# Optimization experiments

Hardware: AMD Instinct MI355X
Metric: run time of the kernel (lower is better)

Reference implementation:

```python
import jax, jax.numpy as jnp
import numpy as np

IN_F, OUT_F, GROUP = 4096, 11008, 128
NUM_GROUPS = IN_F // GROUP


def setup_inputs() -> dict:
    key = jax.random.key(0)
    k1, k2, k3, k4 = jax.random.split(key, 4)
    x = jax.random.normal(k1, (4, 2048, IN_F), dtype=jnp.float32)
    weight_q = jax.random.randint(k2, (OUT_F, IN_F), 0, 127, dtype=jnp.int32)
    scales = jax.random.uniform(k3, (OUT_F, NUM_GROUPS), dtype=jnp.float16) * jnp.float16(0.01)
    bias = jax.random.normal(k4, (OUT_F,), dtype=jnp.float32)
    return {"x": x, "weight_q": weight_q, "scales": scales, "bias": bias}


def _group_dequantize(weight_q, scales):
    # symmetric: W[o, g*G + j] = q[o, g*G + j] * scales[o, g]
    q = weight_q.astype(jnp.float32).reshape(OUT_F, NUM_GROUPS, GROUP)
    w = q * scales.astype(jnp.float32)[:, :, None]
    return w.reshape(OUT_F, IN_F)


def reference(x, weight_q, scales, bias):
    W = _group_dequantize(weight_q, scales).astype(x.dtype)  # [O, I]
    # F.linear: x @ W.T + bias
    out = jnp.einsum('bsi,oi->bso', x, W) + bias.astype(x.dtype)
    return out
```

## Files before the change

### kernel.cpp

```cpp
#include <hip/hip_runtime.h>
#include <hip/hip_fp16.h>

#define K_DIM   4096
#define N_DIM   11008
#define M_DIM   8192
#define NGROUPS 32

#define BM 128
#define BN 128
#define BK 64

typedef __bf16 bf16x8 __attribute__((ext_vector_type(8)));
typedef float  f32x4  __attribute__((ext_vector_type(4)));

#define GAS __attribute__((address_space(1)))
#define LAS __attribute__((address_space(3)))

__device__ __forceinline__ unsigned short f2bf(float f) {
    unsigned int u = __float_as_uint(f);
    u += 0x7fffu + ((u >> 16) & 1u);
    return (unsigned short)(u >> 16);
}

__global__ void prep_x_kernel(const float4* __restrict__ x, ushort4* __restrict__ xb, int nq) {
    int stride = gridDim.x * blockDim.x;
    for (int i = blockIdx.x * blockDim.x + threadIdx.x; i < nq; i += stride) {
        float4 v = x[i];
        ushort4 o;
        o.x = f2bf(v.x); o.y = f2bf(v.y); o.z = f2bf(v.z); o.w = f2bf(v.w);
        xb[i] = o;
    }
}

__global__ void prep_w_kernel(const int4* __restrict__ q, const float* __restrict__ sc,
                              ushort4* __restrict__ wb, int nq) {
    int stride = gridDim.x * blockDim.x;
    for (int i = blockIdx.x * blockDim.x + threadIdx.x; i < nq; i += stride) {
        int4 v = q[i];
        int o = i >> 10;
        int g = (i & 1023) >> 5;
        float s = sc[(o << 5) + g];
        ushort4 w;
        w.x = f2bf((float)v.x * s);
        w.y = f2bf((float)v.y * s);
        w.z = f2bf((float)v.z * s);
        w.w = f2bf((float)v.w * s);
        wb[i] = w;
    }
}

__global__ void gemm_bf16_kernel(const ushort* __restrict__ A, const ushort* __restrict__ B,
                                 const float* __restrict__ bias, float* __restrict__ C) {
    __shared__ __align__(16) ushort sA[BM * BK];
    __shared__ __align__(16) ushort sB[BN * BK];

    const int tid  = threadIdx.x;
    const int lane = tid & 63;
    const int wid  = tid >> 6;
    const int bn   = blockIdx.x;
    const int bm   = blockIdx.y;

    const ushort* Abase = A + (size_t)bm * BM * K_DIM;
    const ushort* Bbase = B + (size_t)bn * BN * K_DIM;

    int g_off[4];
#pragma unroll
    for (int q = 0; q < 4; ++q) {
        int slot = q * 256 + tid;
        int row  = slot >> 3;
        int g    = (slot & 7) ^ (row & 7);
        g_off[q] = row * K_DIM + g * 8;
    }
    const int lds_u = (tid & ~63) * 8;

    f32x4 acc[4][4];
#pragma unroll
    for (int i = 0; i < 4; ++i)
#pragma unroll
        for (int j = 0; j < 4; ++j) {
            acc[i][j][0] = 0.f; acc[i][j][1] = 0.f;
            acc[i][j][2] = 0.f; acc[i][j][3] = 0.f;
        }

    const int mw = (wid & 1) * 64;
    const int nw = (wid >> 1) * 64;

    for (int kt = 0; kt < K_DIM / BK; ++kt) {
        const int kb = kt * BK;
#pragma unroll
        for (int q = 0; q < 4; ++q) {
            __builtin_amdgcn_global_load_lds(
                (GAS const void*)(Abase + kb + g_off[q]),
                (LAS void*)(&sA[q * 2048 + lds_u]), 16, 0, 0);
        }
#pragma unroll
        for (int q = 0; q < 4; ++q) {
            __builtin_amdgcn_global_load_lds(
                (GAS const void*)(Bbase + kb + g_off[q]),
                (LAS void*)(&sB[q * 2048 + lds_u]), 16, 0, 0);
        }
        __syncthreads();

#pragma unroll
        for (int ks = 0; ks < 2; ++ks) {
            bf16x8 af[4], bfr[4];
#pragma unroll
            for (int i = 0; i < 4; ++i) {
                int row = mw + i * 16 + (lane & 15);
                int g   = ks * 4 + (lane >> 4);
                int gp  = g ^ (row & 7);
                af[i] = *(const bf16x8*)&sA[row * BK + gp * 8];
            }
#pragma unroll
            for (int j = 0; j < 4; ++j) {
                int row = nw + j * 16 + (lane & 15);
                int g   = ks * 4 + (lane >> 4);
                int gp  = g ^ (row & 7);
                bfr[j] = *(const bf16x8*)&sB[row * BK + gp * 8];
            }
#pragma unroll
            for (int i = 0; i < 4; ++i)
#pragma unroll
                for (int j = 0; j < 4; ++j)
                    acc[i][j] = __builtin_amdgcn_mfma_f32_16x16x32_bf16(
                        af[i], bfr[j], acc[i][j], 0, 0, 0);
        }
        __syncthreads();
    }

    const int col_l = lane & 15;
    const int row_l = (lane >> 4) * 4;
#pragma unroll
    for (int j = 0; j < 4; ++j) {
        int gcol = bn * BN + nw + j * 16 + col_l;
        float bv = bias[gcol];
#pragma unroll
        for (int i = 0; i < 4; ++i) {
            int grow0 = bm * BM + mw + i * 16 + row_l;
#pragma unroll
            for (int r = 0; r < 4; ++r) {
                C[(size_t)(grow0 + r) * N_DIM + gcol] = acc[i][j][r] + bv;
            }
        }
    }
}

__global__ void naive_kernel(const float* __restrict__ x, const int* __restrict__ q,
                             const float* __restrict__ sc, const float* __restrict__ b,
                             float* __restrict__ out) {
    size_t idx = (size_t)blockIdx.x * blockDim.x + threadIdx.x;
    size_t total = (size_t)M_DIM * N_DIM;
    if (idx >= total) return;
    int m = (int)(idx / N_DIM);
    int n = (int)(idx % N_DIM);
    float acc = 0.f;
    for (int g = 0; g < NGROUPS; ++g) {
        float s = sc[n * NGROUPS + g];
        float p = 0.f;
        for (int k = g * 128; k < g * 128 + 128; ++k)
            p += x[(size_t)m * K_DIM + k] * (float)q[(size_t)n * K_DIM + k];
        acc += p * s;
    }
    out[idx] = acc + b[n];
}

extern "C" void kernel_launch(void* const* d_in, const int* in_sizes, int n_in,
                              void* d_out, int out_size, void* d_ws, size_t ws_size,
                              hipStream_t stream) {
    const float* x  = (const float*)d_in[0];
    const int*   wq = (const int*)d_in[1];
    const float* sc = (const float*)d_in[2];
    const float* bs = (const float*)d_in[3];
    float* out = (float*)d_out;

    const size_t xb_bytes = (size_t)M_DIM * K_DIM * 2;
    const size_t wb_bytes = (size_t)N_DIM * K_DIM * 2;

    if (ws_size < xb_bytes + wb_bytes) {
        size_t total = (size_t)M_DIM * N_DIM;
        int blocks = (int)((total + 255) / 256);
        naive_kernel<<<blocks, 256, 0, stream>>>(x, wq, sc, bs, out);
        return;
    }

    ushort* xb = (ushort*)d_ws;
    ushort* wb = (ushort*)((char*)d_ws + xb_bytes);

    int nq_x = M_DIM * K_DIM / 4;
    int nq_w = N_DIM * K_DIM / 4;
    prep_x_kernel<<<4096, 256, 0, stream>>>((const float4*)x, (ushort4*)xb, nq_x);
    prep_w_kernel<<<8192, 256, 0, stream>>>((const int4*)wq, sc, (ushort4*)wb, nq_w);

    dim3 grid(N_DIM / BN, M_DIM / BM);
    gemm_bf16_kernel<<<grid, 256, 0, stream>>>(xb, wb, bs, out);
}
```

Baseline: 1.503 ms.

## Use 256x256 tiled GEMM with double-buffered LDS and interleaved load/MFMA phases

Replaces the 128x128 single-buffered GEMM with a 256x256 tile run by 512 threads. Global-to-LDS loads for the next K-tiles are issued in quarter-tile stages between MFMA phases, over a double-buffered 128KB LDS, and s_setprio raises priority during the MFMA phases. Block IDs are remapped so consecutive blocks spread across XCDs and share tiles. The goal is to hide global load latency behind compute and raise arithmetic intensity. The cost is large LDS use, which limits occupancy to one block per CU, and a hand-tuned waitcnt/barrier schedule that is fragile.

```diff
diff --git a/kernel.cpp b/kernel.cpp
--- a/kernel.cpp
+++ b/kernel.cpp
@@ -6,9 +6,10 @@
 #define M_DIM   8192
 #define NGROUPS 32
 
-#define BM 128
-#define BN 128
+#define BM 256
+#define BN 256
 #define BK 64
+#define NT (K_DIM / BK)
 
 typedef __bf16 bf16x8 __attribute__((ext_vector_type(8)));
 typedef float  f32x4  __attribute__((ext_vector_type(4)));
@@ -49,94 +50,165 @@
     }
 }
 
-__global__ void gemm_bf16_kernel(const ushort* __restrict__ A, const ushort* __restrict__ B,
-                                 const float* __restrict__ bias, float* __restrict__ C) {
-    __shared__ __align__(16) ushort sA[BM * BK];
-    __shared__ __align__(16) ushort sB[BN * BK];
+
+#define FENCE()     asm volatile("" ::: "memory")
+#define BARRIER()   do { FENCE(); __builtin_amdgcn_s_barrier(); FENCE(); } while (0)
+#define WAITLGKM0() asm volatile("s_waitcnt lgkmcnt(0)" ::: "memory")
+#define WAITVM(n)   asm volatile("s_waitcnt vmcnt(" #n ")" ::: "memory")
+
+#define STAGE(T, H) do {                                                          \
+    const int _b = (T) & 1;                                                       \
+    const ushort* _src;                                                           \
+    ushort* _dst;                                                                 \
+    if ((H) < 2) {                                                                \
+        _src = Abase + (size_t)(H) * 128 * K_DIM + (size_t)(T) * BK;              \
+        _dst = &smem[_b * 16384 + (H) * 8192];                                    \
+    } else {                                                                      \
+        _src = Bbase + (size_t)((H) - 2) * 128 * K_DIM + (size_t)(T) * BK;        \
+        _dst = &smem[32768 + _b * 16384 + ((H) - 2) * 8192];                      \
+    }                                                                             \
+    __builtin_amdgcn_global_load_lds((GAS const void*)(_src + go0),               \
+                                     (LAS void*)(_dst + lds_u), 16, 0, 0);        \
+    __builtin_amdgcn_global_load_lds((GAS const void*)(_src + go1),               \
+                                     (LAS void*)(_dst + 4096 + lds_u), 16, 0, 0); \
+} while (0)
+
+#define READ_A(ABASE) do {                                                        \
+    _Pragma("unroll")                                                             \
+    for (int _i = 0; _i < 8; ++_i) {                                              \
+        af[_i][0] = *(const bf16x8*)&smem[(ABASE) + aA + _i * 1024 + gsw0];       \
+        af[_i][1] = *(const bf16x8*)&smem[(ABASE) + aA + _i * 1024 + gsw1];       \
+    }                                                                             \
+} while (0)
+
+#define READ_B(BBASE, J, BJ) do {                                                 \
+    BJ[0] = *(const bf16x8*)&smem[(BBASE) + bB + (J) * 1024 + gsw0];              \
+    BJ[1] = *(const bf16x8*)&smem[(BBASE) + bB + (J) * 1024 + gsw1];              \
+} while (0)
+
+#define PHASE_MFMA(J, BJ) do {                                                    \
+    __builtin_amdgcn_s_setprio(1);                                                \
+    _Pragma("unroll")                                                             \
+    for (int _ks = 0; _ks < 2; ++_ks) {                                           \
+        _Pragma("unroll")                                                         \
+        for (int _i = 0; _i < 8; ++_i)                                            \
+            acc[_i][J] = __builtin_amdgcn_mfma_f32_16x16x32_bf16(                 \
+                af[_i][_ks], BJ[_ks], acc[_i][J], 0, 0, 0);                       \
+    }                                                                             \
+    __builtin_amdgcn_s_setprio(0);                                                \
+} while (0)
+
+__global__ __launch_bounds__(512, 2)
+void gemm_bf16_256(const ushort* __restrict__ A, const ushort* __restrict__ B,
+                   const float* __restrict__ bias, float* __restrict__ C) {
+    __shared__ __align__(16) ushort smem[65536];
 
     const int tid  = threadIdx.x;
     const int lane = tid & 63;
     const int wid  = tid >> 6;
-    const int bn   = blockIdx.x;
-    const int bm   = blockIdx.y;
+    const int wr   = wid >> 2;
+    const int wc   = wid & 3;
+
+    const int bid  = blockIdx.x;
+    const int wgid = (bid & 7) * 172 + (bid >> 3);
+    const int bm   = wgid & 31;
+    const int bn   = wgid >> 5;
 
     const ushort* Abase = A + (size_t)bm * BM * K_DIM;
     const ushort* Bbase = B + (size_t)bn * BN * K_DIM;
 
-    int g_off[4];
-#pragma unroll
-    for (int q = 0; q < 4; ++q) {
-        int slot = q * 256 + tid;
-        int row  = slot >> 3;
-        int g    = (slot & 7) ^ (row & 7);
-        g_off[q] = row * K_DIM + g * 8;
-    }
+    const int r0  = tid >> 3;
+    const int go0 = r0 * K_DIM + ((tid & 7) ^ (r0 & 7)) * 8;
+    const int s1  = 512 + tid;
+    const int r1  = s1 >> 3;
+    const int go1 = r1 * K_DIM + ((s1 & 7) ^ (r1 & 7)) * 8;
     const int lds_u = (tid & ~63) * 8;
 
-    f32x4 acc[4][4];
-#pragma unroll
-    for (int i = 0; i < 4; ++i)
+    const int aA   = (wr * 128 + (lane & 15)) * 64;
+    const int bB   = (wc * 64  + (lane & 15)) * 64;
+    const int gsw0 = (((lane >> 4))     ^ (lane & 7)) * 8;
+    const int gsw1 = (((lane >> 4) + 4) ^ (lane & 7)) * 8;
+
+    f32x4 acc[8][4];
+#pragma unroll
+    for (int i = 0; i < 8; ++i)
 #pragma unroll
         for (int j = 0; j < 4; ++j) {
             acc[i][j][0] = 0.f; acc[i][j][1] = 0.f;
             acc[i][j][2] = 0.f; acc[i][j][3] = 0.f;
         }
 
-    const int mw = (wid & 1) * 64;
-    const int nw = (wid >> 1) * 64;
-
-    for (int kt = 0; kt < K_DIM / BK; ++kt) {
-        const int kb = kt * BK;
-#pragma unroll
-        for (int q = 0; q < 4; ++q) {
-            __builtin_amdgcn_global_load_lds(
-                (GAS const void*)(Abase + kb + g_off[q]),
-                (LAS void*)(&sA[q * 2048 + lds_u]), 16, 0, 0);
-        }
-#pragma unroll
-        for (int q = 0; q < 4; ++q) {
-            __builtin_amdgcn_global_load_lds(
-                (GAS const void*)(Bbase + kb + g_off[q]),
-                (LAS void*)(&sB[q * 2048 + lds_u]), 16, 0, 0);
-        }
-        __syncthreads();
-
-#pragma unroll
-        for (int ks = 0; ks < 2; ++ks) {
-            bf16x8 af[4], bfr[4];
-#pragma unroll
-            for (int i = 0; i < 4; ++i) {
-                int row = mw + i * 16 + (lane & 15);
-                int g   = ks * 4 + (lane >> 4);
-                int gp  = g ^ (row & 7);
-                af[i] = *(const bf16x8*)&sA[row * BK + gp * 8];
-            }
-#pragma unroll
-            for (int j = 0; j < 4; ++j) {
-                int row = nw + j * 16 + (lane & 15);
-                int g   = ks * 4 + (lane >> 4);
-                int gp  = g ^ (row & 7);
-                bfr[j] = *(const bf16x8*)&sB[row * BK + gp * 8];
-            }
-#pragma unroll
-            for (int i = 0; i < 4; ++i)
-#pragma unroll
-                for (int j = 0; j < 4; ++j)
-                    acc[i][j] = __builtin_amdgcn_mfma_f32_16x16x32_bf16(
-                        af[i], bfr[j], acc[i][j], 0, 0, 0);
-        }
-        __syncthreads();
-    }
+    bf16x8 af[8][2];
+    bf16x8 b0[2], b1[2], b2[2], b3[2];
+
+    STAGE(0, 0); STAGE(0, 1); STAGE(0, 2); STAGE(0, 3);
+    WAITVM(4);
+    STAGE(1, 0); STAGE(1, 1); STAGE(1, 2);
+    WAITVM(6);
+    BARRIER();
+
+    for (int t = 0; t < NT; t += 2) {
+        int t2 = t + 2; if (t2 >= NT) t2 = 0;
+        int t3 = t + 3; if (t3 >= NT) t3 = 1;
+
+        READ_A(0);
+        READ_B(32768, 0, b0);
+        STAGE(t + 1, 3);
+        BARRIER(); WAITLGKM0();
+        PHASE_MFMA(0, b0);
+        BARRIER();
+        READ_B(32768, 1, b1);
+        STAGE(t2, 0);
+        BARRIER(); WAITLGKM0();
+        PHASE_MFMA(1, b1);
+        BARRIER();
+        READ_B(32768, 2, b2);
+        READ_B(32768, 3, b3);
+        STAGE(t2, 1);
+        BARRIER(); WAITLGKM0();
+        PHASE_MFMA(2, b2);
+        BARRIER();
+        STAGE(t2, 2);
+        WAITVM(6);
+        BARRIER();
+        PHASE_MFMA(3, b3);
+        BARRIER();
+
+        READ_A(16384);
+        READ_B(49152, 0, b0);
+        STAGE(t2, 3);
+        BARRIER(); WAITLGKM0();
+        PHASE_MFMA(0, b0);
+        BARRIER();
+        READ_B(49152, 1, b1);
+        STAGE(t3, 0);
+        BARRIER(); WAITLGKM0();
+        PHASE_MFMA(1, b1);
+        BARRIER();
+        READ_B(49152, 2, b2);
+        READ_B(49152, 3, b3);
+        STAGE(t3, 1);
+        BARRIER(); WAITLGKM0();
+        PHASE_MFMA(2, b2);
+        BARRIER();
+        STAGE(t3, 2);
+        WAITVM(6);
+        BARRIER();
+        PHASE_MFMA(3, b3);
+        BARRIER();
+    }
+
+    WAITVM(0);
 
     const int col_l = lane & 15;
     const int row_l = (lane >> 4) * 4;
 #pragma unroll
     for (int j = 0; j < 4; ++j) {
-        int gcol = bn * BN + nw + j * 16 + col_l;
+        int gcol = bn * BN + wc * 64 + j * 16 + col_l;
         float bv = bias[gcol];
 #pragma unroll
-        for (int i = 0; i < 4; ++i) {
-            int grow0 = bm * BM + mw + i * 16 + row_l;
+        for (int i = 0; i < 8; ++i) {
+            int grow0 = bm * BM + wr * 128 + i * 16 + row_l;
 #pragma unroll
             for (int r = 0; r < 4; ++r) {
                 C[(size_t)(grow0 + r) * N_DIM + gcol] = acc[i][j][r] + bv;
@@ -191,6 +263,6 @@
     prep_x_kernel<<<4096, 256, 0, stream>>>((const float4*)x, (ushort4*)xb, nq_x);
     prep_w_kernel<<<8192, 256, 0, stream>>>((const int4*)wq, sc, (ushort4*)wb, nq_w);
 
-    dim3 grid(N_DIM / BN, M_DIM / BM);
-    gemm_bf16_kernel<<<grid, 256, 0, stream>>>(xb, wb, bs, out);
-}
+    dim3 grid((N_DIM / BN) * (M_DIM / BM));
+    gemm_bf16_256<<<grid, 512, 0, stream>>>(xb, wb, bs, out);
+}
```

After: 1.225 ms. 18.5% less time.
